# Performance work log

Hardware: AMD Instinct MI355X
Metric: run time of the kernel (lower is better)

Reference implementation:

```python
import jax, jax.numpy as jnp
import numpy as np

SCALE = 0.02
EPS = 1e-5


def setup_inputs() -> dict:
    key = jax.random.key(0)
    ks = jax.random.split(key, 11)
    C = 256
    inp = {
        "x": jax.random.normal(ks[0], (64, C, 28, 28), dtype=jnp.float32),
        "w1": jax.random.normal(ks[1], (C, C, 3, 3), dtype=jnp.float32) * 0.05,
        "g1": jax.random.uniform(ks[2], (C,), dtype=jnp.float32, minval=0.5, maxval=1.5),
        "b1": jax.random.normal(ks[3], (C,), dtype=jnp.float32) * 0.1,
        "m1": jax.random.normal(ks[4], (C,), dtype=jnp.float32) * 0.1,
        "v1": jax.random.uniform(ks[5], (C,), dtype=jnp.float32, minval=0.5, maxval=1.5),
        "w2": jax.random.normal(ks[6], (C, C, 3, 3), dtype=jnp.float32) * 0.05,
        "g2": jax.random.uniform(ks[7], (C,), dtype=jnp.float32, minval=0.5, maxval=1.5),
        "b2": jax.random.normal(ks[8], (C,), dtype=jnp.float32) * 0.1,
        "m2": jax.random.normal(ks[9], (C,), dtype=jnp.float32) * 0.1,
        "v2": jax.random.uniform(ks[10], (C,), dtype=jnp.float32, minval=0.5, maxval=1.5),
    }
    return inp


def _bin_conv3x3(x, w, stride=1):
    # 1-bit weight conv: sign(w)*scale, straight-through estimator for grads.
    wb = w + jax.lax.stop_gradient(jnp.sign(w) - w)
    y = jax.lax.conv_general_dilated(
        x, wb,
        window_strides=(stride, stride),
        padding=[(1, 1), (1, 1)],
        dimension_numbers=("NCHW", "OIHW", "NCHW"),
    )
    return y * SCALE


def _bn(x, g, b, m, v):
    # eval-mode batchnorm with running stats
    inv = g * jax.lax.rsqrt(v + EPS)  # [C]
    return x * inv[None, :, None, None] + (b - m * inv)[None, :, None, None]


def reference(x, w1, g1, b1, m1, v1, w2, g2, b2, m2, v2):
    out = jax.nn.relu(_bn(_bin_conv3x3(x, w1, 1), g1, b1, m1, v1))
    out = _bn(_bin_conv3x3(out, w2, 1), g2, b2, m2, v2)
    return jax.nn.relu(out + x)
```

## Files before the change

### kernel.cpp

```cpp
#include <hip/hip_runtime.h>

#define EPS_F 1e-5f
#define SCALE_F 0.02f

using short8  = __attribute__((ext_vector_type(8))) short;
using floatx4 = __attribute__((ext_vector_type(4))) float;

__device__ __forceinline__ unsigned short f2bf(float f) {
  unsigned u = __float_as_uint(f);
  return (unsigned short)((u + 0x7fffu + ((u >> 16) & 1u)) >> 16);
}

__global__ void prep_w(const float* __restrict__ w1, const float* __restrict__ w2,
                       unsigned short* __restrict__ ap1, unsigned short* __restrict__ ap2,
                       const float* g1, const float* b1, const float* m1, const float* v1,
                       const float* g2, const float* b2, const float* m2, const float* v2,
                       float* bnp) {
  __shared__ unsigned short sgn[32][289];
  const int tid = threadIdx.x;
  const int bx  = blockIdx.x;
  const int sel = bx >> 6;
  const int tile = bx & 63;
  const int co0 = (tile >> 3) * 32;
  const int ci0 = (tile & 7) * 32;
  const float* __restrict__ w = sel ? w2 : w1;
  unsigned short* __restrict__ ap = sel ? ap2 : ap1;

#pragma unroll
  for (int k = 0; k < 9; ++k) {
    int u = tid + k * 256;
    int co_i = u / 72;
    int rem  = u - co_i * 72;
    const float* src = w + ((size_t)(co0 + co_i) * 256 + ci0) * 9 + rem * 4;
    floatx4 f = *(const floatx4*)src;
#pragma unroll
    for (int q = 0; q < 4; ++q) {
      float v = f[q];
      sgn[co_i][rem * 4 + q] =
          (v > 0.f) ? (unsigned short)0x3F80 : ((v < 0.f) ? (unsigned short)0xBF80 : (unsigned short)0);
    }
  }
  __syncthreads();

  for (int u = tid; u < 1152; u += 256) {
    int co_i = u & 31;
    int c8l  = (u >> 5) & 3;
    int t    = u >> 7;
    short8 o;
#pragma unroll
    for (int j = 0; j < 8; ++j)
      o[j] = (short)sgn[co_i][(c8l * 8 + j) * 9 + t];
    size_t dst = (size_t)(t * 32 + (ci0 >> 3) + c8l) * 2048 + (size_t)(co0 + co_i) * 8;
    *(short8*)(ap + dst) = o;
  }

  if (bx == 0) {
    int c = tid;
    float i1 = g1[c] * rsqrtf(v1[c] + EPS_F);
    bnp[c]       = SCALE_F * i1;
    bnp[256 + c] = b1[c] - m1[c] * i1;
    float i2 = g2[c] * rsqrtf(v2[c] + EPS_F);
    bnp[512 + c] = SCALE_F * i2;
    bnp[768 + c] = b2[c] - m2[c] * i2;
  }
}

__global__ void prep_x(const float* __restrict__ x, unsigned short* __restrict__ xb,
                       unsigned short* __restrict__ abuf) {
  __shared__ unsigned short xt[28 * 264];
  int h = blockIdx.x;
  int n = blockIdx.y;
  int tid = threadIdx.x;

#pragma unroll
  for (int k = 0; k < 7; ++k) {
    int u = tid + k * 256;
    int ci = u / 7;
    int f4 = u - ci * 7;
    const float* src = x + ((size_t)n * 256 + ci) * 784 + h * 28 + f4 * 4;
    floatx4 f = *(const floatx4*)src;
#pragma unroll
    for (int q = 0; q < 4; ++q)
      xt[(f4 * 4 + q) * 264 + ci] = f2bf(f[q]);
  }
  __syncthreads();

  unsigned short* xd = xb + ((size_t)n * 900 + (h + 1) * 30 + 1) * 256;
  for (int u = tid; u < 896; u += 256) {
    int px = u >> 5;
    int c8 = (u & 31) * 8;
    *(short8*)(xd + (size_t)px * 256 + c8) = *(const short8*)&xt[px * 264 + c8];
  }

  {
    int bufi = tid >> 7, side = (tid >> 6) & 1, c4 = tid & 63;
    unsigned short* bb = (bufi ? abuf : xb) + ((size_t)n * 900 + (h + 1) * 30 + side * 29) * 256;
    ushort4 z = {0, 0, 0, 0};
    *(ushort4*)(bb + c4 * 4) = z;
  }
  if (h == 0 || h == 27) {
    int row = (h == 0) ? 0 : 29;
    for (int u = tid; u < 3840; u += 256) {
      int bufi = u / 1920;
      int r    = u - bufi * 1920;
      int px   = r >> 6, c4 = r & 63;
      unsigned short* bb = (bufi ? abuf : xb) + ((size_t)n * 900 + row * 30 + px) * 256;
      ushort4 z = {0, 0, 0, 0};
      *(ushort4*)(bb + c4 * 4) = z;
    }
  }
}

template<int STAGE>
__global__ __launch_bounds__(256, 2) void bconv(
    const unsigned short* __restrict__ Bin,
    const unsigned short* __restrict__ Apack,
    const float* __restrict__ bnp,
    unsigned short* __restrict__ aout,
    const float* __restrict__ xres,
    float* __restrict__ out)
{
  __shared__ __align__(16) unsigned short smem[STAGE == 1 ? 29568 : 24576];

  const int tid  = threadIdx.x;
  const int lane = tid & 63;
  const int wv   = tid >> 6;
  const int quad = lane >> 4;
  const int l16  = lane & 15;

  int flat = blockIdx.y * 7 + blockIdx.x;
  int idx  = (flat & 7) * 56 + (flat >> 3);
  const int n     = idx / 7;
  const int spBlk = idx - n * 7;

  const int prow0 = 4 * spBlk;
  const unsigned short* bsrc = Bin + ((size_t)n * 900 + prow0 * 30) * 256;
  const int coW = wv * 64;

  int pxS[7];
#pragma unroll
  for (int s = 0; s < 7; ++s) {
    int lm = s * 16 + l16;
    int hl = lm / 28;
    int w  = lm - hl * 28;
    pxS[s] = hl * 30 + w;
  }

  int goff0, goff1, goff2, goff3, goff4, goff5;
  {
#define MKGOFF(dst, r) { int v = (r) * 256 + tid; int px = v >> 3; \
    if (px > 179) px = 179; int c = (v & 7) ^ (px & 7); dst = px * 256 + c * 8; }
    MKGOFF(goff0, 0) MKGOFF(goff1, 1) MKGOFF(goff2, 2)
    MKGOFF(goff3, 3) MKGOFF(goff4, 4) MKGOFF(goff5, 5)
#undef MKGOFF
  }

#define STAGE_CB(cbi, bufsel) { \
  unsigned short* lb = smem + (bufsel) * 12288 + wv * 512; \
  const unsigned short* gb = bsrc + (cbi) * 64; \
  __builtin_amdgcn_global_load_lds((const __attribute__((address_space(1))) void*)(gb + goff0), \
      (__attribute__((address_space(3))) void*)(lb + 0 * 2048), 16, 0, 0); \
  __builtin_amdgcn_global_load_lds((const __attribute__((address_space(1))) void*)(gb + goff1), \
      (__attribute__((address_space(3))) void*)(lb + 1 * 2048), 16, 0, 0); \
  __builtin_amdgcn_global_load_lds((const __attribute__((address_space(1))) void*)(gb + goff2), \
      (__attribute__((address_space(3))) void*)(lb + 2 * 2048), 16, 0, 0); \
  __builtin_amdgcn_global_load_lds((const __attribute__((address_space(1))) void*)(gb + goff3), \
      (__attribute__((address_space(3))) void*)(lb + 3 * 2048), 16, 0, 0); \
  __builtin_amdgcn_global_load_lds((const __attribute__((address_space(1))) void*)(gb + goff4), \
      (__attribute__((address_space(3))) void*)(lb + 4 * 2048), 16, 0, 0); \
  __builtin_amdgcn_global_load_lds((const __attribute__((address_space(1))) void*)(gb + goff5), \
      (__attribute__((address_space(3))) void*)(lb + 5 * 2048), 16, 0, 0); }

#define LOADA(d0, d1, d2, d3, t, half, CQ8) { \
  const unsigned short* p = Apack + ((size_t)(((t) * 32 + (CQ8) + (half) * 4) * 256 + coW + l16)) * 8; \
  d0 = *(const short8*)p; \
  d1 = *(const short8*)(p + 16 * 8); \
  d2 = *(const short8*)(p + 32 * 8); \
  d3 = *(const short8*)(p + 48 * 8); }

#define HALFMMA(a0, a1, a2, a3, Cx, Dv) { \
  __builtin_amdgcn_s_setprio(1); \
  _Pragma("unroll") \
  for (int s = 0; s < 7; ++s) { \
    int pe = pxS[s] + (Dv); \
    short8 b = *(const short8*)&Blds[(pe << 6) + (((Cx) ^ (pe & 7)) << 3)]; \
    acc[0][s] = __builtin_amdgcn_mfma_f32_16x16x32_bf16(a0, b, acc[0][s], 0, 0, 0); \
    acc[1][s] = __builtin_amdgcn_mfma_f32_16x16x32_bf16(a1, b, acc[1][s], 0, 0, 0); \
    acc[2][s] = __builtin_amdgcn_mfma_f32_16x16x32_bf16(a2, b, acc[2][s], 0, 0, 0); \
    acc[3][s] = __builtin_amdgcn_mfma_f32_16x16x32_bf16(a3, b, acc[3][s], 0, 0, 0); \
  } \
  __builtin_amdgcn_s_setprio(0); }

  floatx4 acc[4][7];
#pragma unroll
  for (int c = 0; c < 4; ++c)
#pragma unroll
    for (int s = 0; s < 7; ++s)
      acc[c][s] = (floatx4){0.f, 0.f, 0.f, 0.f};

  short8 A0, A1, A2, A3, N0, N1, N2, N3;

  STAGE_CB(0, 0);
  LOADA(A0, A1, A2, A3, 0, 0, quad);
  LOADA(N0, N1, N2, N3, 0, 1, quad);
  __syncthreads();

#pragma unroll 1
  for (int cb = 0; cb < 4; ++cb) {
    unsigned short* Blds = smem + (cb & 1) * 12288;
    if (cb < 3) STAGE_CB(cb + 1, (cb + 1) & 1);
    const int cq8 = cb * 8 + quad;
    int D = 0;
#pragma unroll 1
    for (int t = 0; t < 9; ++t) {
      HALFMMA(A0, A1, A2, A3, quad, D);
      if (t < 8) LOADA(A0, A1, A2, A3, t + 1, 0, cq8);
      HALFMMA(N0, N1, N2, N3, 4 + quad, D);
      if (t < 8) LOADA(N0, N1, N2, N3, t + 1, 1, cq8);
      D += (t == 2 || t == 5) ? 28 : 1;
    }
    if (cb < 3) {
      LOADA(A0, A1, A2, A3, 0, 0, cq8 + 8);
      LOADA(N0, N1, N2, N3, 0, 1, cq8 + 8);
      __syncthreads();
    }
  }

  if (STAGE == 1) {
    __syncthreads();
#pragma unroll
    for (int c = 0; c < 4; ++c) {
      int co = coW + c * 16 + quad * 4;
      floatx4 As = *(const floatx4*)(bnp + co);
      floatx4 Bs = *(const floatx4*)(bnp + 256 + co);
#pragma unroll
      for (int s = 0; s < 7; ++s) {
        int px = s * 16 + l16;
        ushort4 o;
        o.x = f2bf(fmaxf(acc[c][s][0] * As[0] + Bs[0], 0.f));
        o.y = f2bf(fmaxf(acc[c][s][1] * As[1] + Bs[1], 0.f));
        o.z = f2bf(fmaxf(acc[c][s][2] * As[2] + Bs[2], 0.f));
        o.w = f2bf(fmaxf(acc[c][s][3] * As[3] + Bs[3], 0.f));
        *(ushort4*)&smem[px * 264 + co] = o;
      }
    }
    __syncthreads();
    unsigned short* dst0 = aout + ((size_t)n * 900 + (prow0 + 1) * 30 + 1) * 256;
    for (int u = tid; u < 3584; u += 256) {
      int px = u >> 5;
      int c8 = (u & 31) * 8;
      int r  = px / 28;
      int w  = px - r * 28;
      *(short8*)(dst0 + (size_t)(r * 30 + w) * 256 + c8) = *(const short8*)&smem[px * 264 + c8];
    }
  } else {
#pragma unroll
    for (int c = 0; c < 4; ++c) {
      int co = coW + c * 16 + quad * 4;
      floatx4 As = *(const floatx4*)(bnp + 512 + co);
      floatx4 Bs = *(const floatx4*)(bnp + 768 + co);
#pragma unroll
      for (int s = 0; s < 7; ++s) {
        int m = spBlk * 112 + s * 16 + l16;
#pragma unroll
        for (int r = 0; r < 4; ++r) {
          size_t oidx = ((size_t)n * 256 + co + r) * 784 + m;
          float v = acc[c][s][r] * As[r] + Bs[r] + xres[oidx];
          out[oidx] = fmaxf(v, 0.f);
        }
      }
    }
  }
#undef STAGE_CB
#undef LOADA
#undef HALFMMA
}


extern "C" void kernel_launch(void* const* d_in, const int* in_sizes, int n_in,
                              void* d_out, int out_size, void* d_ws, size_t ws_size,
                              hipStream_t stream) {
  const float* x  = (const float*)d_in[0];
  const float* w1 = (const float*)d_in[1];
  const float* g1 = (const float*)d_in[2];
  const float* b1 = (const float*)d_in[3];
  const float* m1 = (const float*)d_in[4];
  const float* v1 = (const float*)d_in[5];
  const float* w2 = (const float*)d_in[6];
  const float* g2 = (const float*)d_in[7];
  const float* b2 = (const float*)d_in[8];
  const float* m2 = (const float*)d_in[9];
  const float* v2 = (const float*)d_in[10];
  float* out = (float*)d_out;

  char* ws = (char*)d_ws;
  const size_t PADBUF = (size_t)64 * 900 * 256 * 2;
  const size_t WPACK  = 589824ull * 2;
  unsigned short* xb   = (unsigned short*)ws;
  unsigned short* abuf = (unsigned short*)(ws + PADBUF);
  unsigned short* ap1  = (unsigned short*)(ws + 2 * PADBUF);
  unsigned short* ap2  = (unsigned short*)(ws + 2 * PADBUF + WPACK);
  float* bnp           = (float*)(ws + 2 * PADBUF + 2 * WPACK);

  prep_w<<<dim3(128), 256, 0, stream>>>(w1, w2, ap1, ap2,
                                        g1, b1, m1, v1, g2, b2, m2, v2, bnp);
  prep_x<<<dim3(28, 64), 256, 0, stream>>>(x, xb, abuf);

  dim3 grid(7, 64);
  bconv<1><<<grid, 256, 0, stream>>>(xb,   ap1, bnp, abuf, nullptr, nullptr);
  bconv<2><<<grid, 256, 0, stream>>>(abuf, ap2, bnp, nullptr, x, out);
}
```

Measured before the change: 229.4 us.

## Split MFMA loop into LDS-read and MMA phases with barrier-synchronized ping-pong

Each half-step now first issues all seven B-fragment LDS reads into registers, then issues the next global A loads, and only then runs the MFMA burst behind an s_barrier and lgkmcnt wait. The global staging for the next channel block and the A-fragment prefetches are moved inside the inner loop so they interleave with compute. The aim is to overlap memory latency with MFMA work and keep waves in lockstep so MFMA bursts alternate. The cost is two extra workgroup barriers per phase and more live registers for the buffered B fragments, which may lower occupancy or stall waves.

```diff
diff --git a/kernel.cpp b/kernel.cpp
--- a/kernel.cpp
+++ b/kernel.cpp
@@ -178,18 +178,27 @@
   d2 = *(const short8*)(p + 32 * 8); \
   d3 = *(const short8*)(p + 48 * 8); }
 
-#define HALFMMA(a0, a1, a2, a3, Cx, Dv) { \
+#define PHASE_BFR(Cx, Dv) { \
+  _Pragma("unroll") \
+  for (int s = 0; s < 7; ++s) { \
+    int pe = pxS[s] + (Dv); \
+    bfr[s] = *(const short8*)&Blds[(pe << 6) + (((Cx) ^ (pe & 7)) << 3)]; \
+  } }
+
+#define PHASE_MMA(a0, a1, a2, a3) { \
+  __builtin_amdgcn_s_barrier(); \
+  asm volatile("s_waitcnt lgkmcnt(0)" ::: "memory"); \
+  __builtin_amdgcn_sched_barrier(0); \
   __builtin_amdgcn_s_setprio(1); \
   _Pragma("unroll") \
   for (int s = 0; s < 7; ++s) { \
-    int pe = pxS[s] + (Dv); \
-    short8 b = *(const short8*)&Blds[(pe << 6) + (((Cx) ^ (pe & 7)) << 3)]; \
-    acc[0][s] = __builtin_amdgcn_mfma_f32_16x16x32_bf16(a0, b, acc[0][s], 0, 0, 0); \
-    acc[1][s] = __builtin_amdgcn_mfma_f32_16x16x32_bf16(a1, b, acc[1][s], 0, 0, 0); \
-    acc[2][s] = __builtin_amdgcn_mfma_f32_16x16x32_bf16(a2, b, acc[2][s], 0, 0, 0); \
-    acc[3][s] = __builtin_amdgcn_mfma_f32_16x16x32_bf16(a3, b, acc[3][s], 0, 0, 0); \
+    acc[0][s] = __builtin_amdgcn_mfma_f32_16x16x32_bf16(a0, bfr[s], acc[0][s], 0, 0, 0); \
+    acc[1][s] = __builtin_amdgcn_mfma_f32_16x16x32_bf16(a1, bfr[s], acc[1][s], 0, 0, 0); \
+    acc[2][s] = __builtin_amdgcn_mfma_f32_16x16x32_bf16(a2, bfr[s], acc[2][s], 0, 0, 0); \
+    acc[3][s] = __builtin_amdgcn_mfma_f32_16x16x32_bf16(a3, bfr[s], acc[3][s], 0, 0, 0); \
   } \
-  __builtin_amdgcn_s_setprio(0); }
+  __builtin_amdgcn_s_setprio(0); \
+  __builtin_amdgcn_s_barrier(); }
 
   floatx4 acc[4][7];
 #pragma unroll
@@ -199,6 +208,7 @@
       acc[c][s] = (floatx4){0.f, 0.f, 0.f, 0.f};
 
   short8 A0, A1, A2, A3, N0, N1, N2, N3;
+  short8 bfr[7];
 
   STAGE_CB(0, 0);
   LOADA(A0, A1, A2, A3, 0, 0, quad);
@@ -208,19 +218,27 @@
 #pragma unroll 1
   for (int cb = 0; cb < 4; ++cb) {
     unsigned short* Blds = smem + (cb & 1) * 12288;
-    if (cb < 3) STAGE_CB(cb + 1, (cb + 1) & 1);
     const int cq8 = cb * 8 + quad;
     int D = 0;
 #pragma unroll 1
     for (int t = 0; t < 9; ++t) {
-      HALFMMA(A0, A1, A2, A3, quad, D);
-      if (t < 8) LOADA(A0, A1, A2, A3, t + 1, 0, cq8);
-      HALFMMA(N0, N1, N2, N3, 4 + quad, D);
-      if (t < 8) LOADA(N0, N1, N2, N3, t + 1, 1, cq8);
+      PHASE_BFR(quad, D);
+      if (t == 0) {
+        if (cb < 3) { STAGE_CB(cb + 1, (cb + 1) & 1); }
+      } else {
+        LOADA(N0, N1, N2, N3, t, 1, cq8);
+      }
+      PHASE_MMA(A0, A1, A2, A3);
+      PHASE_BFR(4 + quad, D);
+      if (t < 8) {
+        LOADA(A0, A1, A2, A3, t + 1, 0, cq8);
+      } else if (cb < 3) {
+        LOADA(A0, A1, A2, A3, 0, 0, cq8 + 8);
+      }
+      PHASE_MMA(N0, N1, N2, N3);
       D += (t == 2 || t == 5) ? 28 : 1;
     }
     if (cb < 3) {
-      LOADA(A0, A1, A2, A3, 0, 0, cq8 + 8);
       LOADA(N0, N1, N2, N3, 0, 1, cq8 + 8);
       __syncthreads();
     }
@@ -273,7 +291,8 @@
   }
 #undef STAGE_CB
 #undef LOADA
-#undef HALFMMA
+#undef PHASE_BFR
+#undef PHASE_MMA
 }
 
 
```

New measurement: 245.6 us. +7.1%, slower.

## Split conv blocks across eight waves and merge weight and input prep kernels

Applied to the files above, without the earlier changes.

Each conv block now runs 512 threads (8 waves), and each wave computes 32 output channels instead of 64. This halves per-wave accumulator and A-fragment registers and raises the number of resident waves to hide latency. The cost is that each B fragment read from LDS now feeds only two MFMAs instead of four, so LDS read traffic per FLOP doubles. Separately, the weight-packing and input-conversion kernels are merged into one launch to save a kernel launch gap.

```diff
diff --git a/kernel.cpp b/kernel.cpp
--- a/kernel.cpp
+++ b/kernel.cpp
@@ -11,108 +11,111 @@
   return (unsigned short)((u + 0x7fffu + ((u >> 16) & 1u)) >> 16);
 }
 
-__global__ void prep_w(const float* __restrict__ w1, const float* __restrict__ w2,
-                       unsigned short* __restrict__ ap1, unsigned short* __restrict__ ap2,
-                       const float* g1, const float* b1, const float* m1, const float* v1,
-                       const float* g2, const float* b2, const float* m2, const float* v2,
-                       float* bnp) {
-  __shared__ unsigned short sgn[32][289];
+__global__ void prep_all(const float* __restrict__ w1, const float* __restrict__ w2,
+                         unsigned short* __restrict__ ap1, unsigned short* __restrict__ ap2,
+                         const float* g1, const float* b1, const float* m1, const float* v1,
+                         const float* g2, const float* b2, const float* m2, const float* v2,
+                         float* bnp,
+                         const float* __restrict__ x, unsigned short* __restrict__ xb,
+                         unsigned short* __restrict__ abuf) {
+  __shared__ __align__(16) unsigned short sh[9248];
+  const int bx  = blockIdx.x;
   const int tid = threadIdx.x;
-  const int bx  = blockIdx.x;
-  const int sel = bx >> 6;
-  const int tile = bx & 63;
-  const int co0 = (tile >> 3) * 32;
-  const int ci0 = (tile & 7) * 32;
-  const float* __restrict__ w = sel ? w2 : w1;
-  unsigned short* __restrict__ ap = sel ? ap2 : ap1;
-
-#pragma unroll
-  for (int k = 0; k < 9; ++k) {
-    int u = tid + k * 256;
-    int co_i = u / 72;
-    int rem  = u - co_i * 72;
-    const float* src = w + ((size_t)(co0 + co_i) * 256 + ci0) * 9 + rem * 4;
-    floatx4 f = *(const floatx4*)src;
-#pragma unroll
-    for (int q = 0; q < 4; ++q) {
-      float v = f[q];
-      sgn[co_i][rem * 4 + q] =
-          (v > 0.f) ? (unsigned short)0x3F80 : ((v < 0.f) ? (unsigned short)0xBF80 : (unsigned short)0);
-    }
-  }
-  __syncthreads();
-
-  for (int u = tid; u < 1152; u += 256) {
-    int co_i = u & 31;
-    int c8l  = (u >> 5) & 3;
-    int t    = u >> 7;
-    short8 o;
-#pragma unroll
-    for (int j = 0; j < 8; ++j)
-      o[j] = (short)sgn[co_i][(c8l * 8 + j) * 9 + t];
-    size_t dst = (size_t)(t * 32 + (ci0 >> 3) + c8l) * 2048 + (size_t)(co0 + co_i) * 8;
-    *(short8*)(ap + dst) = o;
-  }
-
-  if (bx == 0) {
-    int c = tid;
-    float i1 = g1[c] * rsqrtf(v1[c] + EPS_F);
-    bnp[c]       = SCALE_F * i1;
-    bnp[256 + c] = b1[c] - m1[c] * i1;
-    float i2 = g2[c] * rsqrtf(v2[c] + EPS_F);
-    bnp[512 + c] = SCALE_F * i2;
-    bnp[768 + c] = b2[c] - m2[c] * i2;
-  }
-}
-
-__global__ void prep_x(const float* __restrict__ x, unsigned short* __restrict__ xb,
-                       unsigned short* __restrict__ abuf) {
-  __shared__ unsigned short xt[28 * 264];
-  int h = blockIdx.x;
-  int n = blockIdx.y;
-  int tid = threadIdx.x;
-
-#pragma unroll
-  for (int k = 0; k < 7; ++k) {
-    int u = tid + k * 256;
-    int ci = u / 7;
-    int f4 = u - ci * 7;
-    const float* src = x + ((size_t)n * 256 + ci) * 784 + h * 28 + f4 * 4;
-    floatx4 f = *(const floatx4*)src;
-#pragma unroll
-    for (int q = 0; q < 4; ++q)
-      xt[(f4 * 4 + q) * 264 + ci] = f2bf(f[q]);
-  }
-  __syncthreads();
-
-  unsigned short* xd = xb + ((size_t)n * 900 + (h + 1) * 30 + 1) * 256;
-  for (int u = tid; u < 896; u += 256) {
-    int px = u >> 5;
-    int c8 = (u & 31) * 8;
-    *(short8*)(xd + (size_t)px * 256 + c8) = *(const short8*)&xt[px * 264 + c8];
-  }
-
-  {
-    int bufi = tid >> 7, side = (tid >> 6) & 1, c4 = tid & 63;
-    unsigned short* bb = (bufi ? abuf : xb) + ((size_t)n * 900 + (h + 1) * 30 + side * 29) * 256;
-    ushort4 z = {0, 0, 0, 0};
-    *(ushort4*)(bb + c4 * 4) = z;
-  }
-  if (h == 0 || h == 27) {
-    int row = (h == 0) ? 0 : 29;
-    for (int u = tid; u < 3840; u += 256) {
-      int bufi = u / 1920;
-      int r    = u - bufi * 1920;
-      int px   = r >> 6, c4 = r & 63;
-      unsigned short* bb = (bufi ? abuf : xb) + ((size_t)n * 900 + row * 30 + px) * 256;
+
+  if (bx < 128) {
+    unsigned short (*sgn)[289] = (unsigned short (*)[289])sh;
+    const int sel = bx >> 6;
+    const int tile = bx & 63;
+    const int co0 = (tile >> 3) * 32;
+    const int ci0 = (tile & 7) * 32;
+    const float* __restrict__ w = sel ? w2 : w1;
+    unsigned short* __restrict__ ap = sel ? ap2 : ap1;
+
+#pragma unroll
+    for (int k = 0; k < 9; ++k) {
+      int u = tid + k * 256;
+      int co_i = u / 72;
+      int rem  = u - co_i * 72;
+      const float* src = w + ((size_t)(co0 + co_i) * 256 + ci0) * 9 + rem * 4;
+      floatx4 f = *(const floatx4*)src;
+#pragma unroll
+      for (int q = 0; q < 4; ++q) {
+        float v = f[q];
+        sgn[co_i][rem * 4 + q] =
+            (v > 0.f) ? (unsigned short)0x3F80 : ((v < 0.f) ? (unsigned short)0xBF80 : (unsigned short)0);
+      }
+    }
+    __syncthreads();
+
+    for (int u = tid; u < 1152; u += 256) {
+      int co_i = u & 31;
+      int c8l  = (u >> 5) & 3;
+      int t    = u >> 7;
+      short8 o;
+#pragma unroll
+      for (int j = 0; j < 8; ++j)
+        o[j] = (short)sgn[co_i][(c8l * 8 + j) * 9 + t];
+      size_t dst = (size_t)(t * 32 + (ci0 >> 3) + c8l) * 2048 + (size_t)(co0 + co_i) * 8;
+      *(short8*)(ap + dst) = o;
+    }
+
+    if (bx == 0) {
+      int c = tid;
+      float i1 = g1[c] * rsqrtf(v1[c] + EPS_F);
+      bnp[c]       = SCALE_F * i1;
+      bnp[256 + c] = b1[c] - m1[c] * i1;
+      float i2 = g2[c] * rsqrtf(v2[c] + EPS_F);
+      bnp[512 + c] = SCALE_F * i2;
+      bnp[768 + c] = b2[c] - m2[c] * i2;
+    }
+  } else {
+    unsigned short* xt = sh;
+    int p = bx - 128;
+    int h = p % 28;
+    int n = p / 28;
+
+#pragma unroll
+    for (int k = 0; k < 7; ++k) {
+      int u = tid + k * 256;
+      int ci = u / 7;
+      int f4 = u - ci * 7;
+      const float* src = x + ((size_t)n * 256 + ci) * 784 + h * 28 + f4 * 4;
+      floatx4 f = *(const floatx4*)src;
+#pragma unroll
+      for (int q = 0; q < 4; ++q)
+        xt[(f4 * 4 + q) * 264 + ci] = f2bf(f[q]);
+    }
+    __syncthreads();
+
+    unsigned short* xd = xb + ((size_t)n * 900 + (h + 1) * 30 + 1) * 256;
+    for (int u = tid; u < 896; u += 256) {
+      int px = u >> 5;
+      int c8 = (u & 31) * 8;
+      *(short8*)(xd + (size_t)px * 256 + c8) = *(const short8*)&xt[px * 264 + c8];
+    }
+
+    {
+      int bufi = tid >> 7, side = (tid >> 6) & 1, c4 = tid & 63;
+      unsigned short* bb = (bufi ? abuf : xb) + ((size_t)n * 900 + (h + 1) * 30 + side * 29) * 256;
       ushort4 z = {0, 0, 0, 0};
       *(ushort4*)(bb + c4 * 4) = z;
     }
+    if (h == 0 || h == 27) {
+      int row = (h == 0) ? 0 : 29;
+      for (int u = tid; u < 3840; u += 256) {
+        int bufi = u / 1920;
+        int r    = u - bufi * 1920;
+        int px   = r >> 6, c4 = r & 63;
+        unsigned short* bb = (bufi ? abuf : xb) + ((size_t)n * 900 + row * 30 + px) * 256;
+        ushort4 z = {0, 0, 0, 0};
+        *(ushort4*)(bb + c4 * 4) = z;
+      }
+    }
   }
 }
 
 template<int STAGE>
-__global__ __launch_bounds__(256, 2) void bconv(
+__global__ __launch_bounds__(512, 4) void bconv(
     const unsigned short* __restrict__ Bin,
     const unsigned short* __restrict__ Apack,
     const float* __restrict__ bnp,
@@ -135,7 +138,7 @@
 
   const int prow0 = 4 * spBlk;
   const unsigned short* bsrc = Bin + ((size_t)n * 900 + prow0 * 30) * 256;
-  const int coW = wv * 64;
+  const int coW = wv * 32;
 
   int pxS[7];
 #pragma unroll
@@ -146,12 +149,11 @@
     pxS[s] = hl * 30 + w;
   }
 
-  int goff0, goff1, goff2, goff3, goff4, goff5;
+  int goff0, goff1, goff2;
   {
-#define MKGOFF(dst, r) { int v = (r) * 256 + tid; int px = v >> 3; \
+#define MKGOFF(dst, r) { int v = (r) * 512 + tid; int px = v >> 3; \
     if (px > 179) px = 179; int c = (v & 7) ^ (px & 7); dst = px * 256 + c * 8; }
     MKGOFF(goff0, 0) MKGOFF(goff1, 1) MKGOFF(goff2, 2)
-    MKGOFF(goff3, 3) MKGOFF(goff4, 4) MKGOFF(goff5, 5)
 #undef MKGOFF
   }
 
@@ -159,26 +161,18 @@
   unsigned short* lb = smem + (bufsel) * 12288 + wv * 512; \
   const unsigned short* gb = bsrc + (cbi) * 64; \
   __builtin_amdgcn_global_load_lds((const __attribute__((address_space(1))) void*)(gb + goff0), \
-      (__attribute__((address_space(3))) void*)(lb + 0 * 2048), 16, 0, 0); \
+      (__attribute__((address_space(3))) void*)(lb + 0 * 4096), 16, 0, 0); \
   __builtin_amdgcn_global_load_lds((const __attribute__((address_space(1))) void*)(gb + goff1), \
-      (__attribute__((address_space(3))) void*)(lb + 1 * 2048), 16, 0, 0); \
+      (__attribute__((address_space(3))) void*)(lb + 1 * 4096), 16, 0, 0); \
   __builtin_amdgcn_global_load_lds((const __attribute__((address_space(1))) void*)(gb + goff2), \
-      (__attribute__((address_space(3))) void*)(lb + 2 * 2048), 16, 0, 0); \
-  __builtin_amdgcn_global_load_lds((const __attribute__((address_space(1))) void*)(gb + goff3), \
-      (__attribute__((address_space(3))) void*)(lb + 3 * 2048), 16, 0, 0); \
-  __builtin_amdgcn_global_load_lds((const __attribute__((address_space(1))) void*)(gb + goff4), \
-      (__attribute__((address_space(3))) void*)(lb + 4 * 2048), 16, 0, 0); \
-  __builtin_amdgcn_global_load_lds((const __attribute__((address_space(1))) void*)(gb + goff5), \
-      (__attribute__((address_space(3))) void*)(lb + 5 * 2048), 16, 0, 0); }
-
-#define LOADA(d0, d1, d2, d3, t, half, CQ8) { \
+      (__attribute__((address_space(3))) void*)(lb + 2 * 4096), 16, 0, 0); }
+
+#define LOADA2(d0, d1, t, half, CQ8) { \
   const unsigned short* p = Apack + ((size_t)(((t) * 32 + (CQ8) + (half) * 4) * 256 + coW + l16)) * 8; \
   d0 = *(const short8*)p; \
-  d1 = *(const short8*)(p + 16 * 8); \
-  d2 = *(const short8*)(p + 32 * 8); \
-  d3 = *(const short8*)(p + 48 * 8); }
-
-#define HALFMMA(a0, a1, a2, a3, Cx, Dv) { \
+  d1 = *(const short8*)(p + 16 * 8); }
+
+#define HALFMMA2(a0, a1, Cx, Dv) { \
   __builtin_amdgcn_s_setprio(1); \
   _Pragma("unroll") \
   for (int s = 0; s < 7; ++s) { \
@@ -186,42 +180,40 @@
     short8 b = *(const short8*)&Blds[(pe << 6) + (((Cx) ^ (pe & 7)) << 3)]; \
     acc[0][s] = __builtin_amdgcn_mfma_f32_16x16x32_bf16(a0, b, acc[0][s], 0, 0, 0); \
     acc[1][s] = __builtin_amdgcn_mfma_f32_16x16x32_bf16(a1, b, acc[1][s], 0, 0, 0); \
-    acc[2][s] = __builtin_amdgcn_mfma_f32_16x16x32_bf16(a2, b, acc[2][s], 0, 0, 0); \
-    acc[3][s] = __builtin_amdgcn_mfma_f32_16x16x32_bf16(a3, b, acc[3][s], 0, 0, 0); \
   } \
   __builtin_amdgcn_s_setprio(0); }
 
-  floatx4 acc[4][7];
-#pragma unroll
-  for (int c = 0; c < 4; ++c)
+  floatx4 acc[2][7];
+#pragma unroll
+  for (int c = 0; c < 2; ++c)
 #pragma unroll
     for (int s = 0; s < 7; ++s)
       acc[c][s] = (floatx4){0.f, 0.f, 0.f, 0.f};
 
-  short8 A0, A1, A2, A3, N0, N1, N2, N3;
+  short8 A0, A1, N0, N1;
 
   STAGE_CB(0, 0);
-  LOADA(A0, A1, A2, A3, 0, 0, quad);
-  LOADA(N0, N1, N2, N3, 0, 1, quad);
+  LOADA2(A0, A1, 0, 0, quad);
+  LOADA2(N0, N1, 0, 1, quad);
   __syncthreads();
 
 #pragma unroll 1
   for (int cb = 0; cb < 4; ++cb) {
     unsigned short* Blds = smem + (cb & 1) * 12288;
-    if (cb < 3) STAGE_CB(cb + 1, (cb + 1) & 1);
+    if (cb < 3) { STAGE_CB(cb + 1, (cb + 1) & 1); }
     const int cq8 = cb * 8 + quad;
     int D = 0;
 #pragma unroll 1
     for (int t = 0; t < 9; ++t) {
-      HALFMMA(A0, A1, A2, A3, quad, D);
-      if (t < 8) LOADA(A0, A1, A2, A3, t + 1, 0, cq8);
-      HALFMMA(N0, N1, N2, N3, 4 + quad, D);
-      if (t < 8) LOADA(N0, N1, N2, N3, t + 1, 1, cq8);
+      HALFMMA2(A0, A1, quad, D);
+      if (t < 8) { LOADA2(A0, A1, t + 1, 0, cq8); }
+      HALFMMA2(N0, N1, 4 + quad, D);
+      if (t < 8) { LOADA2(N0, N1, t + 1, 1, cq8); }
       D += (t == 2 || t == 5) ? 28 : 1;
     }
     if (cb < 3) {
-      LOADA(A0, A1, A2, A3, 0, 0, cq8 + 8);
-      LOADA(N0, N1, N2, N3, 0, 1, cq8 + 8);
+      LOADA2(A0, A1, 0, 0, cq8 + 8);
+      LOADA2(N0, N1, 0, 1, cq8 + 8);
       __syncthreads();
     }
   }
@@ -229,7 +221,7 @@
   if (STAGE == 1) {
     __syncthreads();
 #pragma unroll
-    for (int c = 0; c < 4; ++c) {
+    for (int c = 0; c < 2; ++c) {
       int co = coW + c * 16 + quad * 4;
       floatx4 As = *(const floatx4*)(bnp + co);
       floatx4 Bs = *(const floatx4*)(bnp + 256 + co);
@@ -246,7 +238,7 @@
     }
     __syncthreads();
     unsigned short* dst0 = aout + ((size_t)n * 900 + (prow0 + 1) * 30 + 1) * 256;
-    for (int u = tid; u < 3584; u += 256) {
+    for (int u = tid; u < 3584; u += 512) {
       int px = u >> 5;
       int c8 = (u & 31) * 8;
       int r  = px / 28;
@@ -255,7 +247,7 @@
     }
   } else {
 #pragma unroll
-    for (int c = 0; c < 4; ++c) {
+    for (int c = 0; c < 2; ++c) {
       int co = coW + c * 16 + quad * 4;
       floatx4 As = *(const floatx4*)(bnp + 512 + co);
       floatx4 Bs = *(const floatx4*)(bnp + 768 + co);
@@ -272,8 +264,8 @@
     }
   }
 #undef STAGE_CB
-#undef LOADA
-#undef HALFMMA
+#undef LOADA2
+#undef HALFMMA2
 }
 
 
@@ -302,11 +294,11 @@
   unsigned short* ap2  = (unsigned short*)(ws + 2 * PADBUF + WPACK);
   float* bnp           = (float*)(ws + 2 * PADBUF + 2 * WPACK);
 
-  prep_w<<<dim3(128), 256, 0, stream>>>(w1, w2, ap1, ap2,
-                                        g1, b1, m1, v1, g2, b2, m2, v2, bnp);
-  prep_x<<<dim3(28, 64), 256, 0, stream>>>(x, xb, abuf);
+  prep_all<<<dim3(1920), 256, 0, stream>>>(w1, w2, ap1, ap2,
+                                           g1, b1, m1, v1, g2, b2, m2, v2, bnp,
+                                           x, xb, abuf);
 
   dim3 grid(7, 64);
-  bconv<1><<<grid, 256, 0, stream>>>(xb,   ap1, bnp, abuf, nullptr, nullptr);
-  bconv<2><<<grid, 256, 0, stream>>>(abuf, ap2, bnp, nullptr, x, out);
+  bconv<1><<<grid, 512, 0, stream>>>(xb,   ap1, bnp, abuf, nullptr, nullptr);
+  bconv<2><<<grid, 512, 0, stream>>>(abuf, ap2, bnp, nullptr, x, out);
 }
```

After: 223.2 us. 2.7% less time.
